# Kernel tuning notes

Hardware: AMD Instinct MI355X
Metric: run time of the kernel (lower is better)

Reference implementation:

```python
import jax, jax.numpy as jnp
import numpy as np

BLOCK_SIZE = 64

def quantize_dequantize(w, block_size=BLOCK_SIZE):
    # LPBQ double quantization: block-wise abs-max -> uint4 scale1 over fp32 scale2
    out_ch, in_ch = w.shape
    pad_len = (block_size - in_ch % block_size) % block_size
    if pad_len > 0:
        w = jnp.pad(w, ((0, 0), (0, pad_len)))
    wr = w.reshape(out_ch, -1, block_size)                      # [O, nB, B]
    s1 = jnp.clip(jnp.max(jnp.abs(wr), axis=-1, keepdims=True) / 7.0, 1e-8)   # [O, nB, 1]
    s2 = jnp.clip(jnp.max(s1, axis=1, keepdims=True) / 15.0, 1e-8)            # [O, 1, 1]
    s1_q = jnp.clip(jnp.round(s1 / s2), 0.0, 15.0)
    s1_recon = s1_q * s2
    w_q = jnp.clip(jnp.round(wr / s1_recon), -8.0, 7.0)
    w_recon = (w_q * s1_recon).reshape(out_ch, -1)
    if pad_len > 0:
        w_recon = w_recon[:, :-pad_len]
    return w_recon

def setup_inputs() -> dict:
    key = jax.random.key(0)
    k1, k2, k3 = jax.random.split(key, 3)
    B, S, IN, OUT = 1, 128, 4096, 11008
    x = jax.random.normal(k1, (B, S, IN), dtype=jnp.float32)
    weight = jax.random.normal(k2, (OUT, IN), dtype=jnp.float32)
    bias = jax.random.normal(k3, (OUT,), dtype=jnp.float32)
    return {"x": x, "weight": weight, "bias": bias}

def reference(x, weight, bias):
    w_q = quantize_dequantize(weight)
    # F.linear: x @ w_q.T + bias
    return jnp.einsum('bsi,oi->bso', x, w_q) + bias
```

## Files before the change

### kernel.cpp

```cpp
#include <hip/hip_runtime.h>
#include <hip/hip_bf16.h>

#define IN_CH 4096
#define OUT_CH 11008
#define QBLK 64

#define BM 128
#define BN 64
#define BK 64
#define KCHUNKS (IN_CH / BK)
#define KSPLIT 4
#define SPLIT_CHUNKS (KCHUNKS / KSPLIT)
#define NTILES (OUT_CH / BN)
#define XCONV_BLOCKS 16

typedef short bf16x8 __attribute__((ext_vector_type(8)));
typedef float f32x4 __attribute__((ext_vector_type(4)));

#define GLOBAL_AS __attribute__((address_space(1)))
#define LDS_AS __attribute__((address_space(3)))

__device__ inline unsigned short f2bf(float f) {
    union { __hip_bfloat16 h; unsigned short u; } cv;
    cv.h = __float2bfloat16(f);
    return cv.u;
}

__global__ __launch_bounds__(256) void quant_kernel(
        const float* __restrict__ w, const float* __restrict__ x,
        unsigned short* __restrict__ wq, unsigned short* __restrict__ xq) {
    const int tid = threadIdx.x;

    if (blockIdx.x >= OUT_CH) {
        const int bx = blockIdx.x - OUT_CH;
        const float4* x4 = (const float4*)x;
        for (int it = 0; it < 32; ++it) {
            const int g = bx * 8192 + it * 256 + tid;
            float4 v = x4[g];
            ushort4 o;
            o.x = f2bf(v.x); o.y = f2bf(v.y); o.z = f2bf(v.z); o.w = f2bf(v.w);
            ((ushort4*)xq)[g] = o;
        }
        return;
    }

    const float* wrow = w + (size_t)blockIdx.x * IN_CH;
    unsigned short* orow = wq + (size_t)blockIdx.x * IN_CH;

    __shared__ float s1_lds[64];
    __shared__ float s2_lds;

    float4 v[4];
    const int lane16 = tid & 15;

    for (int p = 0; p < 4; ++p) {
        v[p] = ((const float4*)wrow)[p * 256 + tid];
        float m = fmaxf(fmaxf(fabsf(v[p].x), fabsf(v[p].y)),
                        fmaxf(fabsf(v[p].z), fabsf(v[p].w)));
        m = fmaxf(m, __shfl_xor(m, 1));
        m = fmaxf(m, __shfl_xor(m, 2));
        m = fmaxf(m, __shfl_xor(m, 4));
        m = fmaxf(m, __shfl_xor(m, 8));
        if (lane16 == 0)
            s1_lds[p * 16 + (tid >> 4)] = fmaxf(m * (1.0f / 7.0f), 1e-8f);
    }
    __syncthreads();

    if (tid < 64) {
        float m = s1_lds[tid];
        m = fmaxf(m, __shfl_xor(m, 1));
        m = fmaxf(m, __shfl_xor(m, 2));
        m = fmaxf(m, __shfl_xor(m, 4));
        m = fmaxf(m, __shfl_xor(m, 8));
        m = fmaxf(m, __shfl_xor(m, 16));
        m = fmaxf(m, __shfl_xor(m, 32));
        if (tid == 0) s2_lds = fmaxf(m * (1.0f / 15.0f), 1e-8f);
    }
    __syncthreads();
    const float s2 = s2_lds;

    for (int p = 0; p < 4; ++p) {
        const float s1 = s1_lds[p * 16 + (tid >> 4)];
        const float s1q = fminf(fmaxf(rintf(s1 / s2), 0.0f), 15.0f);
        const float s1r = s1q * s2;
        ushort4 o;
        o.x = f2bf(fminf(fmaxf(rintf(v[p].x / s1r), -8.0f), 7.0f) * s1r);
        o.y = f2bf(fminf(fmaxf(rintf(v[p].y / s1r), -8.0f), 7.0f) * s1r);
        o.z = f2bf(fminf(fmaxf(rintf(v[p].z / s1r), -8.0f), 7.0f) * s1r);
        o.w = f2bf(fminf(fmaxf(rintf(v[p].w / s1r), -8.0f), 7.0f) * s1r);
        ((ushort4*)orow)[p * 256 + tid] = o;
    }
}

__global__ __launch_bounds__(256) void gemm_kernel(
        const unsigned short* __restrict__ A, const unsigned short* __restrict__ B,
        float* __restrict__ part) {
    __shared__ __align__(16) unsigned short ldsA[BM * BK];
    __shared__ __align__(16) unsigned short ldsB[BN * BK];

    const int tid = threadIdx.x;
    const int w = tid >> 6;
    const int l = tid & 63;
    const int wm = w >> 1;
    const int wn = w & 1;
    const int n0 = blockIdx.x * BN;
    const int kc0 = blockIdx.y * SPLIT_CHUNKS;

    const int r8 = l >> 3;
    const int sg = l & 7;

    f32x4 acc[4][2] = {};

    const int lane15 = l & 15;
    const int quad = l >> 4;

    for (int kc = kc0; kc < kc0 + SPLIT_CHUNKS; ++kc) {
        const int k0 = kc * BK;

        for (int i = 0; i < 4; ++i) {
            const int r = i * 32 + w * 8 + r8;
            const unsigned short* gp = A + (size_t)r * IN_CH + k0 + sg * 8;
            LDS_AS unsigned short* lp =
                (LDS_AS unsigned short*)&ldsA[(i * 32 + w * 8) * BK];
            __builtin_amdgcn_global_load_lds((const GLOBAL_AS void*)gp,
                                             (LDS_AS void*)lp, 16, 0, 0);
        }
        for (int j = 0; j < 2; ++j) {
            const int r = j * 32 + w * 8 + r8;
            const unsigned short* gp = B + (size_t)(n0 + r) * IN_CH + k0 + sg * 8;
            LDS_AS unsigned short* lp =
                (LDS_AS unsigned short*)&ldsB[(j * 32 + w * 8) * BK];
            __builtin_amdgcn_global_load_lds((const GLOBAL_AS void*)gp,
                                             (LDS_AS void*)lp, 16, 0, 0);
        }
        asm volatile("s_waitcnt vmcnt(0)" ::: "memory");
        __syncthreads();

        for (int kk = 0; kk < 2; ++kk) {
            bf16x8 af[4], bfv[2];
            const int ko = kk * 32 + quad * 8;
            for (int i = 0; i < 4; ++i)
                af[i] = *(const bf16x8*)&ldsA[(wm * 64 + i * 16 + lane15) * BK + ko];
            for (int j = 0; j < 2; ++j)
                bfv[j] = *(const bf16x8*)&ldsB[(wn * 32 + j * 16 + lane15) * BK + ko];
            for (int i = 0; i < 4; ++i)
                for (int j = 0; j < 2; ++j)
                    acc[i][j] = __builtin_amdgcn_mfma_f32_16x16x32_bf16(
                        af[i], bfv[j], acc[i][j], 0, 0, 0);
        }
        __syncthreads();
    }

    float* pbase = part + (size_t)blockIdx.y * BM * OUT_CH;
    const int m_base = wm * 64 + quad * 4;
    const int n_base = n0 + wn * 32 + lane15;
    for (int j = 0; j < 2; ++j) {
        for (int i = 0; i < 4; ++i) {
            const int m = m_base + i * 16;
            float* cp = pbase + (size_t)m * OUT_CH + n_base + j * 16;
            cp[0 * OUT_CH] = acc[i][j][0];
            cp[1 * OUT_CH] = acc[i][j][1];
            cp[2 * OUT_CH] = acc[i][j][2];
            cp[3 * OUT_CH] = acc[i][j][3];
        }
    }
}

__global__ __launch_bounds__(256) void reduce_kernel(
        const float* __restrict__ part, const float* __restrict__ bias,
        float* __restrict__ out) {
    const int m = blockIdx.y;
    const int x4 = blockIdx.x * 256 + threadIdx.x;
    if (x4 >= OUT_CH / 4) return;
    const size_t off = (size_t)m * OUT_CH + x4 * 4;

    float4 acc = ((const float4*)bias)[x4];
    for (int s = 0; s < KSPLIT; ++s) {
        float4 p = *(const float4*)(part + (size_t)s * BM * OUT_CH + off);
        acc.x += p.x; acc.y += p.y; acc.z += p.z; acc.w += p.w;
    }
    *(float4*)(out + off) = acc;
}

extern "C" void kernel_launch(void* const* d_in, const int* in_sizes, int n_in,
                              void* d_out, int out_size, void* d_ws, size_t ws_size,
                              hipStream_t stream) {
    const float* x = (const float*)d_in[0];
    const float* weight = (const float*)d_in[1];
    const float* bias = (const float*)d_in[2];
    float* out = (float*)d_out;

    unsigned short* wsW = (unsigned short*)d_ws;
    unsigned short* wsX = wsW + (size_t)OUT_CH * IN_CH;
    float* wsP = (float*)(wsX + (size_t)BM * IN_CH);

    quant_kernel<<<OUT_CH + XCONV_BLOCKS, 256, 0, stream>>>(weight, x, wsW, wsX);
    gemm_kernel<<<dim3(NTILES, KSPLIT), 256, 0, stream>>>(wsX, wsW, wsP);
    reduce_kernel<<<dim3((OUT_CH / 4 + 255) / 256, BM), 256, 0, stream>>>(
        wsP, bias, out);
}
```

Baseline: 300.8 us.

## Store quantized weights as int8 with scales and dequantize in GEMM

The quant kernel now writes int8 weight codes plus a transposed per-block scale array instead of fully dequantized bf16 weights. This halves the weight bytes written and re-read by the GEMM. The GEMM loads the int8 codes with regular vector loads, multiplies by the scale, converts to bf16 and stores into a padded LDS tile. The trade-off is extra ALU and conversion work in the GEMM inner loop, and the B operand loses the async direct-to-LDS load path.

```diff
diff --git a/kernel.cpp b/kernel.cpp
--- a/kernel.cpp
+++ b/kernel.cpp
@@ -13,9 +13,11 @@
 #define SPLIT_CHUNKS (KCHUNKS / KSPLIT)
 #define NTILES (OUT_CH / BN)
 #define XCONV_BLOCKS 16
+#define BPAD 72
 
 typedef short bf16x8 __attribute__((ext_vector_type(8)));
 typedef float f32x4 __attribute__((ext_vector_type(4)));
+typedef char char16v __attribute__((ext_vector_type(16)));
 
 #define GLOBAL_AS __attribute__((address_space(1)))
 #define LDS_AS __attribute__((address_space(3)))
@@ -28,7 +30,8 @@
 
 __global__ __launch_bounds__(256) void quant_kernel(
         const float* __restrict__ w, const float* __restrict__ x,
-        unsigned short* __restrict__ wq, unsigned short* __restrict__ xq) {
+        signed char* __restrict__ wq, float* __restrict__ s1rT,
+        unsigned short* __restrict__ xq) {
     const int tid = threadIdx.x;
 
     if (blockIdx.x >= OUT_CH) {
@@ -44,8 +47,9 @@
         return;
     }
 
-    const float* wrow = w + (size_t)blockIdx.x * IN_CH;
-    unsigned short* orow = wq + (size_t)blockIdx.x * IN_CH;
+    const int row = blockIdx.x;
+    const float* wrow = w + (size_t)row * IN_CH;
+    signed char* orow = wq + (size_t)row * IN_CH;
 
     __shared__ float s1_lds[64];
     __shared__ float s2_lds;
@@ -67,36 +71,38 @@
     __syncthreads();
 
     if (tid < 64) {
-        float m = s1_lds[tid];
+        float s1 = s1_lds[tid];
+        float m = s1;
         m = fmaxf(m, __shfl_xor(m, 1));
         m = fmaxf(m, __shfl_xor(m, 2));
         m = fmaxf(m, __shfl_xor(m, 4));
         m = fmaxf(m, __shfl_xor(m, 8));
         m = fmaxf(m, __shfl_xor(m, 16));
         m = fmaxf(m, __shfl_xor(m, 32));
-        if (tid == 0) s2_lds = fmaxf(m * (1.0f / 15.0f), 1e-8f);
-    }
-    __syncthreads();
-    const float s2 = s2_lds;
-
-    for (int p = 0; p < 4; ++p) {
-        const float s1 = s1_lds[p * 16 + (tid >> 4)];
+        const float s2 = fmaxf(m * (1.0f / 15.0f), 1e-8f);
         const float s1q = fminf(fmaxf(rintf(s1 / s2), 0.0f), 15.0f);
         const float s1r = s1q * s2;
-        ushort4 o;
-        o.x = f2bf(fminf(fmaxf(rintf(v[p].x / s1r), -8.0f), 7.0f) * s1r);
-        o.y = f2bf(fminf(fmaxf(rintf(v[p].y / s1r), -8.0f), 7.0f) * s1r);
-        o.z = f2bf(fminf(fmaxf(rintf(v[p].z / s1r), -8.0f), 7.0f) * s1r);
-        o.w = f2bf(fminf(fmaxf(rintf(v[p].w / s1r), -8.0f), 7.0f) * s1r);
-        ((ushort4*)orow)[p * 256 + tid] = o;
+        s1_lds[tid] = s1r;
+        s1rT[(size_t)tid * OUT_CH + row] = s1r;
+    }
+    __syncthreads();
+
+    for (int p = 0; p < 4; ++p) {
+        const float s1r = s1_lds[p * 16 + (tid >> 4)];
+        char4 o;
+        o.x = (signed char)(int)fminf(fmaxf(rintf(v[p].x / s1r), -8.0f), 7.0f);
+        o.y = (signed char)(int)fminf(fmaxf(rintf(v[p].y / s1r), -8.0f), 7.0f);
+        o.z = (signed char)(int)fminf(fmaxf(rintf(v[p].z / s1r), -8.0f), 7.0f);
+        o.w = (signed char)(int)fminf(fmaxf(rintf(v[p].w / s1r), -8.0f), 7.0f);
+        ((char4*)orow)[p * 256 + tid] = o;
     }
 }
 
 __global__ __launch_bounds__(256) void gemm_kernel(
-        const unsigned short* __restrict__ A, const unsigned short* __restrict__ B,
-        float* __restrict__ part) {
+        const unsigned short* __restrict__ A, const signed char* __restrict__ WQ,
+        const float* __restrict__ s1rT, float* __restrict__ part) {
     __shared__ __align__(16) unsigned short ldsA[BM * BK];
-    __shared__ __align__(16) unsigned short ldsB[BN * BK];
+    __shared__ __align__(16) unsigned short ldsB[BN * BPAD];
 
     const int tid = threadIdx.x;
     const int w = tid >> 6;
@@ -109,6 +115,9 @@
     const int r8 = l >> 3;
     const int sg = l & 7;
 
+    const int brow = tid >> 2;
+    const int bcg = tid & 3;
+
     f32x4 acc[4][2] = {};
 
     const int lane15 = l & 15;
@@ -118,21 +127,25 @@
         const int k0 = kc * BK;
 
         for (int i = 0; i < 4; ++i) {
-            const int r = i * 32 + w * 8 + r8;
-            const unsigned short* gp = A + (size_t)r * IN_CH + k0 + sg * 8;
+            const unsigned short* gp =
+                A + (size_t)(i * 32 + w * 8 + r8) * IN_CH + k0 + sg * 8;
             LDS_AS unsigned short* lp =
                 (LDS_AS unsigned short*)&ldsA[(i * 32 + w * 8) * BK];
             __builtin_amdgcn_global_load_lds((const GLOBAL_AS void*)gp,
                                              (LDS_AS void*)lp, 16, 0, 0);
         }
-        for (int j = 0; j < 2; ++j) {
-            const int r = j * 32 + w * 8 + r8;
-            const unsigned short* gp = B + (size_t)(n0 + r) * IN_CH + k0 + sg * 8;
-            LDS_AS unsigned short* lp =
-                (LDS_AS unsigned short*)&ldsB[(j * 32 + w * 8) * BK];
-            __builtin_amdgcn_global_load_lds((const GLOBAL_AS void*)gp,
-                                             (LDS_AS void*)lp, 16, 0, 0);
-        }
+
+        const float s1 = s1rT[(size_t)kc * OUT_CH + n0 + brow];
+        char16v bq = *(const char16v*)(WQ + (size_t)(n0 + brow) * IN_CH +
+                                       k0 + bcg * 16);
+        bf16x8 o0, o1;
+        for (int i = 0; i < 8; ++i)
+            o0[i] = (short)f2bf((float)bq[i] * s1);
+        for (int i = 0; i < 8; ++i)
+            o1[i] = (short)f2bf((float)bq[8 + i] * s1);
+        *(bf16x8*)&ldsB[brow * BPAD + bcg * 16] = o0;
+        *(bf16x8*)&ldsB[brow * BPAD + bcg * 16 + 8] = o1;
+
         asm volatile("s_waitcnt vmcnt(0)" ::: "memory");
         __syncthreads();
 
@@ -142,7 +155,7 @@
             for (int i = 0; i < 4; ++i)
                 af[i] = *(const bf16x8*)&ldsA[(wm * 64 + i * 16 + lane15) * BK + ko];
             for (int j = 0; j < 2; ++j)
-                bfv[j] = *(const bf16x8*)&ldsB[(wn * 32 + j * 16 + lane15) * BK + ko];
+                bfv[j] = *(const bf16x8*)&ldsB[(wn * 32 + j * 16 + lane15) * BPAD + ko];
             for (int i = 0; i < 4; ++i)
                 for (int j = 0; j < 2; ++j)
                     acc[i][j] = __builtin_amdgcn_mfma_f32_16x16x32_bf16(
@@ -190,12 +203,13 @@
     const float* bias = (const float*)d_in[2];
     float* out = (float*)d_out;
 
-    unsigned short* wsW = (unsigned short*)d_ws;
-    unsigned short* wsX = wsW + (size_t)OUT_CH * IN_CH;
-    float* wsP = (float*)(wsX + (size_t)BM * IN_CH);
-
-    quant_kernel<<<OUT_CH + XCONV_BLOCKS, 256, 0, stream>>>(weight, x, wsW, wsX);
-    gemm_kernel<<<dim3(NTILES, KSPLIT), 256, 0, stream>>>(wsX, wsW, wsP);
+    signed char* wsQ = (signed char*)d_ws;
+    unsigned short* wsX = (unsigned short*)(wsQ + (size_t)OUT_CH * IN_CH);
+    float* wsS = (float*)(wsX + (size_t)BM * IN_CH);
+    float* wsP = wsS + (size_t)QBLK * OUT_CH;
+
+    quant_kernel<<<OUT_CH + XCONV_BLOCKS, 256, 0, stream>>>(weight, x, wsQ, wsS, wsX);
+    gemm_kernel<<<dim3(NTILES, KSPLIT), 256, 0, stream>>>(wsX, wsQ, wsS, wsP);
     reduce_kernel<<<dim3((OUT_CH / 4 + 255) / 256, BM), 256, 0, stream>>>(
         wsP, bias, out);
 }
```

New measurement: 297.7 us. No clear change (-1.0%).
